# Optimization experiments

Hardware: AMD Instinct MI355X
Metric: run time of the kernel (lower is better)

## Reference

```python
import jax, jax.numpy as jnp
import numpy as np

N = 100000
E = 1600000
F_IN = 32
HID = 16


def _sage_conv(x, src, dst, W_l, b_l, W_r):
    # PyG SAGEConv (aggr='mean', normalize=False, root_weight=True):
    #   out = lin_l(mean_{j in N(i)} x_j) + lin_r(x_i)
    # lin_l has bias, lin_r has no bias.
    n = x.shape[0]
    msg_sum = jax.ops.segment_sum(x[src], dst, num_segments=n)          # [N, d]
    deg = jax.ops.segment_sum(jnp.ones_like(dst, dtype=x.dtype), dst, num_segments=n)
    agg = msg_sum / jnp.maximum(deg, 1.0)[:, None]                      # mean, 0 for isolated nodes
    return agg @ W_l.T + b_l + x @ W_r.T


def setup_inputs() -> dict:
    key = jax.random.key(0)
    ks = jax.random.split(key, 8)
    x = jax.random.normal(ks[0], (N, F_IN), dtype=jnp.float32)
    edge_index = jax.random.randint(ks[1], (1, 2, E), 0, N, dtype=jnp.int64)
    s1 = 1.0 / np.sqrt(F_IN)
    s2 = 1.0 / np.sqrt(HID)
    W1_l = jax.random.uniform(ks[2], (HID, F_IN), jnp.float32, -s1, s1)
    b1_l = jax.random.uniform(ks[3], (HID,), jnp.float32, -s1, s1)
    W1_r = jax.random.uniform(ks[4], (HID, F_IN), jnp.float32, -s1, s1)
    W2_l = jax.random.uniform(ks[5], (F_IN, HID), jnp.float32, -s2, s2)
    b2_l = jax.random.uniform(ks[6], (F_IN,), jnp.float32, -s2, s2)
    W2_r = jax.random.uniform(ks[7], (F_IN, HID), jnp.float32, -s2, s2)
    return {"x": x, "edge_index": edge_index, "W1_l": W1_l, "b1_l": b1_l,
            "W1_r": W1_r, "W2_l": W2_l, "b2_l": b2_l, "W2_r": W2_r}


def reference(x, edge_index, W1_l, b1_l, W1_r, W2_l, b2_l, W2_r):
    ei = jnp.squeeze(edge_index, axis=0)  # [2, E]
    src, dst = ei[0], ei[1]
    h = jax.nn.relu(_sage_conv(x, src, dst, W1_l, b1_l, W1_r))
    out = _sage_conv(h, src, dst, W2_l, b2_l, W2_r)
    return out
```

## Files before the change

kernel.cpp:

```cpp
#include <hip/hip_runtime.h>

#define F_IN 32
#define HID 16
#define BSHIFT 7
#define BNODES (1 << BSHIFT)
#define CAP 2560
#define CHUNK 8192
#define SRCM 0x1FFFFu
#define WS1 33
#define WS2 17

__device__ __forceinline__ void add4(float4& a, const float4& b) {
    a.x += b.x; a.y += b.y; a.z += b.z; a.w += b.w;
}
__device__ __forceinline__ unsigned pack2(float a, float b) {
    unsigned ua = __float_as_uint(a);
    unsigned ub = __float_as_uint(b);
    ua = (ua + 0x7FFFu + ((ua >> 16) & 1u)) >> 16;
    ub = (ub + 0x7FFFu + ((ub >> 16) & 1u)) >> 16;
    return ua | (ub << 16);
}
__device__ __forceinline__ float lo2f(unsigned u) { return __uint_as_float(u << 16); }
__device__ __forceinline__ float hi2f(unsigned u) { return __uint_as_float(u & 0xFFFF0000u); }
__device__ __forceinline__ float4 unp(uint2 v) {
    return make_float4(lo2f(v.x), hi2f(v.x), lo2f(v.y), hi2f(v.y));
}

__global__ void __launch_bounds__(256) k_pre(const float* __restrict__ x,
                                             const float* __restrict__ W1_l,
                                             unsigned* __restrict__ y1b,
                                             const int* __restrict__ ei,
                                             int* __restrict__ bucketCursor,
                                             unsigned* __restrict__ bucketBuf,
                                             int N, int E, int nodeBlocks) {
    __shared__ int cnt[1024];
    __shared__ int runBase[1024];
    __shared__ float Ws[HID * F_IN];
    int tid = threadIdx.x;

    if ((int)blockIdx.x < nodeBlocks) {
        for (int i = tid; i < HID * F_IN; i += 256) Ws[i] = W1_l[i];
        __syncthreads();
        int node = blockIdx.x * 256 + tid;
        if (node >= N) return;
        float xr[F_IN];
        const float4* xp = (const float4*)(x + (size_t)node * F_IN);
#pragma unroll
        for (int i = 0; i < F_IN / 4; i++) {
            float4 v = xp[i];
            xr[4 * i + 0] = v.x; xr[4 * i + 1] = v.y;
            xr[4 * i + 2] = v.z; xr[4 * i + 3] = v.w;
        }
        float a[HID];
#pragma unroll
        for (int o = 0; o < HID; o++) {
            float s = 0.f;
#pragma unroll
            for (int k = 0; k < F_IN; k++) s += xr[k] * Ws[o * F_IN + k];
            a[o] = s;
        }
        uint4* yp = (uint4*)(y1b + (size_t)node * 8);
        yp[0] = make_uint4(pack2(a[0], a[1]), pack2(a[2], a[3]),
                           pack2(a[4], a[5]), pack2(a[6], a[7]));
        yp[1] = make_uint4(pack2(a[8], a[9]), pack2(a[10], a[11]),
                           pack2(a[12], a[13]), pack2(a[14], a[15]));
        return;
    }

    int pb = blockIdx.x - nodeBlocks;
    int e0 = pb * CHUNK;
    int e1 = min(e0 + CHUNK, E);
    int n4 = (e1 - e0) >> 2;
    const int4* dst4 = (const int4*)(ei + E + e0);
    const int4* src4 = (const int4*)(ei + e0);

#pragma unroll
    for (int i = 0; i < 4; i++) cnt[tid + 256 * i] = 0;
    __syncthreads();
    for (int i = tid; i < n4; i += 256) {
        int4 d = dst4[i];
        atomicAdd(&cnt[d.x >> BSHIFT], 1);
        atomicAdd(&cnt[d.y >> BSHIFT], 1);
        atomicAdd(&cnt[d.z >> BSHIFT], 1);
        atomicAdd(&cnt[d.w >> BSHIFT], 1);
    }
    __syncthreads();
#pragma unroll
    for (int i = 0; i < 4; i++) {
        int b = tid + 256 * i;
        int c = cnt[b];
        runBase[b] = c ? atomicAdd(&bucketCursor[b], c) : 0;
        cnt[b] = 0;
    }
    __syncthreads();
    for (int i = tid; i < n4; i += 256) {
        int4 d = dst4[i];
        int4 s = src4[i];
        {
            int b = d.x >> BSHIFT;
            int pos = runBase[b] + atomicAdd(&cnt[b], 1);
            if (pos < CAP)
                bucketBuf[(size_t)b * CAP + pos] = ((unsigned)(d.x & (BNODES - 1)) << 17) | (unsigned)s.x;
        }
        {
            int b = d.y >> BSHIFT;
            int pos = runBase[b] + atomicAdd(&cnt[b], 1);
            if (pos < CAP)
                bucketBuf[(size_t)b * CAP + pos] = ((unsigned)(d.y & (BNODES - 1)) << 17) | (unsigned)s.y;
        }
        {
            int b = d.z >> BSHIFT;
            int pos = runBase[b] + atomicAdd(&cnt[b], 1);
            if (pos < CAP)
                bucketBuf[(size_t)b * CAP + pos] = ((unsigned)(d.z & (BNODES - 1)) << 17) | (unsigned)s.z;
        }
        {
            int b = d.w >> BSHIFT;
            int pos = runBase[b] + atomicAdd(&cnt[b], 1);
            if (pos < CAP)
                bucketBuf[(size_t)b * CAP + pos] = ((unsigned)(d.w & (BNODES - 1)) << 17) | (unsigned)s.w;
        }
    }
}

__global__ void __launch_bounds__(256) k_agg1f(const unsigned* __restrict__ y1b,
                                               const float* __restrict__ x,
                                               const unsigned* __restrict__ bucketBuf,
                                               const int* __restrict__ bucketCursor,
                                               const float* __restrict__ W1_r,
                                               const float* __restrict__ b1,
                                               unsigned* __restrict__ hb, int N) {
    __shared__ unsigned sA[CAP];
    __shared__ unsigned sB[CAP];
    __shared__ int hist[BNODES];
    __shared__ int scn[BNODES];
    __shared__ int cur[BNODES];
    __shared__ float Ws[HID * WS1];
    __shared__ float bs[HID];
    int tid = threadIdx.x, b = blockIdx.x;

    for (int i = tid; i < HID * F_IN; i += 256) Ws[(i >> 5) * WS1 + (i & 31)] = W1_r[i];
    if (tid < HID) bs[tid] = b1[tid];
    if (tid < BNODES) hist[tid] = 0;
    int nRec = min(bucketCursor[b], CAP);
    const unsigned* buf = bucketBuf + (size_t)b * CAP;
    for (int i = tid; i < nRec; i += 256) sA[i] = buf[i];
    __syncthreads();
    for (int i = tid; i < nRec; i += 256) atomicAdd(&hist[sA[i] >> 17], 1);
    __syncthreads();
    if (tid < BNODES) scn[tid] = hist[tid];
    __syncthreads();
    for (int off = 1; off < BNODES; off <<= 1) {
        int v = (tid < BNODES && tid >= off) ? scn[tid - off] : 0;
        __syncthreads();
        if (tid < BNODES && tid >= off) scn[tid] += v;
        __syncthreads();
    }
    if (tid < BNODES) cur[tid] = scn[tid] - hist[tid];
    __syncthreads();
    for (int i = tid; i < nRec; i += 256) {
        unsigned r = sA[i];
        int pos = atomicAdd(&cur[r >> 17], 1);
        sB[pos] = r & SRCM;
    }
    __syncthreads();

    const uint2* yv = (const uint2*)y1b;
#pragma unroll
    for (int pass = 0; pass < 2; pass++) {
        int slot = pass * 256 + tid;
        int nl = slot >> 2, c = slot & 3;
        int node = b * BNODES + nl;
        if (node >= N) continue;
        int start = scn[nl] - hist[nl];
        int dg = hist[nl];
        int jend = start + dg;
        float4 a0 = make_float4(0, 0, 0, 0), a1 = a0;
        int j = start;
        for (; j + 4 <= jend; j += 4) {
            unsigned s0 = sB[j], s1 = sB[j + 1], s2 = sB[j + 2], s3 = sB[j + 3];
            uint2 v0 = yv[(size_t)s0 * 4 + c];
            uint2 v1 = yv[(size_t)s1 * 4 + c];
            uint2 v2 = yv[(size_t)s2 * 4 + c];
            uint2 v3 = yv[(size_t)s3 * 4 + c];
            add4(a0, unp(v0)); add4(a1, unp(v1));
            add4(a0, unp(v2)); add4(a1, unp(v3));
        }
        for (; j < jend; j++) {
            uint2 v = yv[(size_t)sB[j] * 4 + c];
            add4(a0, unp(v));
        }
        add4(a0, a1);
        float inv = 1.0f / (float)(dg > 0 ? dg : 1);
        float m[4] = {a0.x * inv, a0.y * inv, a0.z * inv, a0.w * inv};

        float xr[F_IN];
        const float4* xp = (const float4*)(x + (size_t)node * F_IN);
#pragma unroll
        for (int q = 0; q < F_IN / 4; q++) {
            float4 v = xp[q];
            xr[4 * q + 0] = v.x; xr[4 * q + 1] = v.y;
            xr[4 * q + 2] = v.z; xr[4 * q + 3] = v.w;
        }
        float a[4];
#pragma unroll
        for (int jj = 0; jj < 4; jj++) {
            int o = c * 4 + jj;
            float s = m[jj] + bs[o];
#pragma unroll
            for (int k = 0; k < F_IN; k++) s += xr[k] * Ws[o * WS1 + k];
            a[jj] = fmaxf(s, 0.0f);
        }
        ((uint2*)hb)[(size_t)node * 4 + c] = make_uint2(pack2(a[0], a[1]), pack2(a[2], a[3]));
    }
}

__global__ void __launch_bounds__(256) k_l2f(const unsigned* __restrict__ hb,
                                             const unsigned* __restrict__ bucketBuf,
                                             const int* __restrict__ bucketCursor,
                                             const float* __restrict__ W2_l,
                                             const float* __restrict__ b2,
                                             const float* __restrict__ W2_r,
                                             float* __restrict__ out, int N) {
    __shared__ unsigned sA[CAP];
    __shared__ unsigned sB[CAP];
    __shared__ int hist[BNODES];
    __shared__ int scn[BNODES];
    __shared__ int cur[BNODES];
    __shared__ float Wl[F_IN * WS2];
    __shared__ float Wr[F_IN * WS2];
    __shared__ float bs[F_IN];
    int tid = threadIdx.x, b = blockIdx.x;

    for (int i = tid; i < F_IN * HID; i += 256) {
        int r = i >> 4, q = i & 15;
        Wl[r * WS2 + q] = W2_l[i];
        Wr[r * WS2 + q] = W2_r[i];
    }
    if (tid < F_IN) bs[tid] = b2[tid];
    if (tid < BNODES) hist[tid] = 0;
    int nRec = min(bucketCursor[b], CAP);
    const unsigned* buf = bucketBuf + (size_t)b * CAP;
    for (int i = tid; i < nRec; i += 256) sA[i] = buf[i];
    __syncthreads();
    for (int i = tid; i < nRec; i += 256) atomicAdd(&hist[sA[i] >> 17], 1);
    __syncthreads();
    if (tid < BNODES) scn[tid] = hist[tid];
    __syncthreads();
    for (int off = 1; off < BNODES; off <<= 1) {
        int v = (tid < BNODES && tid >= off) ? scn[tid - off] : 0;
        __syncthreads();
        if (tid < BNODES && tid >= off) scn[tid] += v;
        __syncthreads();
    }
    if (tid < BNODES) cur[tid] = scn[tid] - hist[tid];
    __syncthreads();
    for (int i = tid; i < nRec; i += 256) {
        unsigned r = sA[i];
        int pos = atomicAdd(&cur[r >> 17], 1);
        sB[pos] = r & SRCM;
    }
    __syncthreads();

    float* mm = (float*)sA;
    const uint2* hv = (const uint2*)hb;
#pragma unroll
    for (int pass = 0; pass < 2; pass++) {
        int slot = pass * 256 + tid;
        int nl = slot >> 2, c = slot & 3;
        int node = b * BNODES + nl;
        if (node >= N) continue;
        int start = scn[nl] - hist[nl];
        int dg = hist[nl];
        int jend = start + dg;
        float4 a0 = make_float4(0, 0, 0, 0), a1 = a0;
        int j = start;
        for (; j + 4 <= jend; j += 4) {
            unsigned s0 = sB[j], s1 = sB[j + 1], s2 = sB[j + 2], s3 = sB[j + 3];
            uint2 v0 = hv[(size_t)s0 * 4 + c];
            uint2 v1 = hv[(size_t)s1 * 4 + c];
            uint2 v2 = hv[(size_t)s2 * 4 + c];
            uint2 v3 = hv[(size_t)s3 * 4 + c];
            add4(a0, unp(v0)); add4(a1, unp(v1));
            add4(a0, unp(v2)); add4(a1, unp(v3));
        }
        for (; j < jend; j++) {
            uint2 v = hv[(size_t)sB[j] * 4 + c];
            add4(a0, unp(v));
        }
        add4(a0, a1);
        float inv = 1.0f / (float)(dg > 0 ? dg : 1);
        mm[nl * (HID + 1) + c * 4 + 0] = a0.x * inv;
        mm[nl * (HID + 1) + c * 4 + 1] = a0.y * inv;
        mm[nl * (HID + 1) + c * 4 + 2] = a0.z * inv;
        mm[nl * (HID + 1) + c * 4 + 3] = a0.w * inv;
    }
    __syncthreads();

#pragma unroll
    for (int pass = 0; pass < 2; pass++) {
        int slot = pass * 256 + tid;
        int nl = slot >> 2, c = slot & 3;
        int node = b * BNODES + nl;
        if (node >= N) continue;

        float m[HID];
#pragma unroll
        for (int k = 0; k < HID; k++) m[k] = mm[nl * (HID + 1) + k];

        float hr[HID];
        const uint4* hp = (const uint4*)(hb + (size_t)node * 8);
        uint4 u0 = hp[0], u1 = hp[1];
        hr[0] = lo2f(u0.x); hr[1] = hi2f(u0.x); hr[2] = lo2f(u0.y); hr[3] = hi2f(u0.y);
        hr[4] = lo2f(u0.z); hr[5] = hi2f(u0.z); hr[6] = lo2f(u0.w); hr[7] = hi2f(u0.w);
        hr[8] = lo2f(u1.x); hr[9] = hi2f(u1.x); hr[10] = lo2f(u1.y); hr[11] = hi2f(u1.y);
        hr[12] = lo2f(u1.z); hr[13] = hi2f(u1.z); hr[14] = lo2f(u1.w); hr[15] = hi2f(u1.w);

        float a[8];
#pragma unroll
        for (int jj = 0; jj < 8; jj++) {
            int o = c * 8 + jj;
            float s = bs[o];
#pragma unroll
            for (int k = 0; k < HID; k++)
                s += m[k] * Wl[o * WS2 + k] + hr[k] * Wr[o * WS2 + k];
            a[jj] = s;
        }
        float4* op = (float4*)(out + (size_t)node * F_IN + c * 8);
        op[0] = make_float4(a[0], a[1], a[2], a[3]);
        op[1] = make_float4(a[4], a[5], a[6], a[7]);
    }
}

extern "C" void kernel_launch(void* const* d_in, const int* in_sizes, int n_in,
                              void* d_out, int out_size, void* d_ws, size_t ws_size,
                              hipStream_t stream) {
    const float* x    = (const float*)d_in[0];
    const int*   ei   = (const int*)d_in[1];
    const float* W1_l = (const float*)d_in[2];
    const float* b1   = (const float*)d_in[3];
    const float* W1_r = (const float*)d_in[4];
    const float* W2_l = (const float*)d_in[5];
    const float* b2   = (const float*)d_in[6];
    const float* W2_r = (const float*)d_in[7];
    float* out = (float*)d_out;

    const int N = in_sizes[0] / F_IN;
    const int E = in_sizes[1] / 2;
    const int nbuckets = (N + BNODES - 1) >> BSHIFT;

    int* bucketCursor = (int*)d_ws;
    unsigned* bucketBuf = (unsigned*)(bucketCursor + 1024);
    unsigned* y1b = bucketBuf + (size_t)nbuckets * CAP;
    unsigned* hb  = y1b + (size_t)N * 8;

    hipMemsetAsync(bucketCursor, 0, 1024 * sizeof(int), stream);

    const int nodeBlocks = (N + 255) / 256;
    const int partBlocks = (E + CHUNK - 1) / CHUNK;

    k_pre<<<nodeBlocks + partBlocks, 256, 0, stream>>>(x, W1_l, y1b, ei,
                                                       bucketCursor, bucketBuf,
                                                       N, E, nodeBlocks);
    k_agg1f<<<nbuckets, 256, 0, stream>>>(y1b, x, bucketBuf, bucketCursor,
                                          W1_r, b1, hb, N);
    k_l2f<<<nbuckets, 256, 0, stream>>>(hb, bucketBuf, bucketCursor,
                                        W2_l, b2, W2_r, out, N);
}
```

Before: 159.9 us.

## Reuse layer-1 CSR sort in layer 2, split dense matvecs across lanes, unroll gathers

```diff
diff --git a/kernel.cpp b/kernel.cpp
--- a/kernel.cpp
+++ b/kernel.cpp
@@ -5,7 +5,7 @@
 #define BSHIFT 7
 #define BNODES (1 << BSHIFT)
 #define CAP 2560
-#define CHUNK 8192
+#define CHUNK 4096
 #define SRCM 0x1FFFFu
 #define WS1 33
 #define WS2 17
@@ -125,8 +125,9 @@
 
 __global__ void __launch_bounds__(256) k_agg1f(const unsigned* __restrict__ y1b,
                                                const float* __restrict__ x,
-                                               const unsigned* __restrict__ bucketBuf,
+                                               unsigned* __restrict__ bucketBuf,
                                                const int* __restrict__ bucketCursor,
+                                               unsigned* __restrict__ rdPacked,
                                                const float* __restrict__ W1_r,
                                                const float* __restrict__ b1,
                                                unsigned* __restrict__ hb, int N) {
@@ -143,7 +144,7 @@
     if (tid < HID) bs[tid] = b1[tid];
     if (tid < BNODES) hist[tid] = 0;
     int nRec = min(bucketCursor[b], CAP);
-    const unsigned* buf = bucketBuf + (size_t)b * CAP;
+    unsigned* buf = bucketBuf + (size_t)b * CAP;
     for (int i = tid; i < nRec; i += 256) sA[i] = buf[i];
     __syncthreads();
     for (int i = tid; i < nRec; i += 256) atomicAdd(&hist[sA[i] >> 17], 1);
@@ -164,6 +165,13 @@
         sB[pos] = r & SRCM;
     }
     __syncthreads();
+
+    for (int i = tid; i < nRec; i += 256) buf[i] = sB[i];
+    if (tid < BNODES) {
+        int node = b * BNODES + tid;
+        if (node < N)
+            rdPacked[node] = ((unsigned)(scn[tid] - hist[tid]) << 16) | (unsigned)hist[tid];
+    }
 
     const uint2* yv = (const uint2*)y1b;
 #pragma unroll
@@ -175,41 +183,53 @@
         int start = scn[nl] - hist[nl];
         int dg = hist[nl];
         int jend = start + dg;
-        float4 a0 = make_float4(0, 0, 0, 0), a1 = a0;
+        float4 a0 = make_float4(0, 0, 0, 0), a1 = a0, a2 = a0, a3 = a0;
         int j = start;
-        for (; j + 4 <= jend; j += 4) {
+        for (; j + 8 <= jend; j += 8) {
             unsigned s0 = sB[j], s1 = sB[j + 1], s2 = sB[j + 2], s3 = sB[j + 3];
+            unsigned s4 = sB[j + 4], s5 = sB[j + 5], s6 = sB[j + 6], s7 = sB[j + 7];
             uint2 v0 = yv[(size_t)s0 * 4 + c];
             uint2 v1 = yv[(size_t)s1 * 4 + c];
             uint2 v2 = yv[(size_t)s2 * 4 + c];
             uint2 v3 = yv[(size_t)s3 * 4 + c];
-            add4(a0, unp(v0)); add4(a1, unp(v1));
-            add4(a0, unp(v2)); add4(a1, unp(v3));
+            uint2 v4 = yv[(size_t)s4 * 4 + c];
+            uint2 v5 = yv[(size_t)s5 * 4 + c];
+            uint2 v6 = yv[(size_t)s6 * 4 + c];
+            uint2 v7 = yv[(size_t)s7 * 4 + c];
+            add4(a0, unp(v0)); add4(a1, unp(v1)); add4(a2, unp(v2)); add4(a3, unp(v3));
+            add4(a0, unp(v4)); add4(a1, unp(v5)); add4(a2, unp(v6)); add4(a3, unp(v7));
         }
         for (; j < jend; j++) {
             uint2 v = yv[(size_t)sB[j] * 4 + c];
             add4(a0, unp(v));
         }
-        add4(a0, a1);
+        add4(a0, a1); add4(a2, a3); add4(a0, a2);
         float inv = 1.0f / (float)(dg > 0 ? dg : 1);
         float m[4] = {a0.x * inv, a0.y * inv, a0.z * inv, a0.w * inv};
 
-        float xr[F_IN];
-        const float4* xp = (const float4*)(x + (size_t)node * F_IN);
-#pragma unroll
-        for (int q = 0; q < F_IN / 4; q++) {
-            float4 v = xp[q];
-            xr[4 * q + 0] = v.x; xr[4 * q + 1] = v.y;
-            xr[4 * q + 2] = v.z; xr[4 * q + 3] = v.w;
+        float xq[8];
+        const float4* xp = (const float4*)(x + (size_t)node * F_IN + c * 8);
+        float4 va = xp[0], vb = xp[1];
+        xq[0] = va.x; xq[1] = va.y; xq[2] = va.z; xq[3] = va.w;
+        xq[4] = vb.x; xq[5] = vb.y; xq[6] = vb.z; xq[7] = vb.w;
+        float p[HID];
+#pragma unroll
+        for (int o = 0; o < HID; o++) {
+            float s = 0.f;
+#pragma unroll
+            for (int k = 0; k < 8; k++) s += xq[k] * Ws[o * WS1 + c * 8 + k];
+            p[o] = s;
+        }
+#pragma unroll
+        for (int o = 0; o < HID; o++) {
+            p[o] += __shfl_xor(p[o], 1);
+            p[o] += __shfl_xor(p[o], 2);
         }
         float a[4];
 #pragma unroll
         for (int jj = 0; jj < 4; jj++) {
             int o = c * 4 + jj;
-            float s = m[jj] + bs[o];
-#pragma unroll
-            for (int k = 0; k < F_IN; k++) s += xr[k] * Ws[o * WS1 + k];
-            a[jj] = fmaxf(s, 0.0f);
+            a[jj] = fmaxf(m[jj] + bs[o] + p[o], 0.0f);
         }
         ((uint2*)hb)[(size_t)node * 4 + c] = make_uint2(pack2(a[0], a[1]), pack2(a[2], a[3]));
     }
@@ -218,15 +238,14 @@
 __global__ void __launch_bounds__(256) k_l2f(const unsigned* __restrict__ hb,
                                              const unsigned* __restrict__ bucketBuf,
                                              const int* __restrict__ bucketCursor,
+                                             const unsigned* __restrict__ rdPacked,
                                              const float* __restrict__ W2_l,
                                              const float* __restrict__ b2,
                                              const float* __restrict__ W2_r,
                                              float* __restrict__ out, int N) {
-    __shared__ unsigned sA[CAP];
     __shared__ unsigned sB[CAP];
-    __shared__ int hist[BNODES];
-    __shared__ int scn[BNODES];
-    __shared__ int cur[BNODES];
+    __shared__ float mm[BNODES * (HID + 1)];
+    __shared__ unsigned rdS[BNODES];
     __shared__ float Wl[F_IN * WS2];
     __shared__ float Wr[F_IN * WS2];
     __shared__ float bs[F_IN];
@@ -238,31 +257,15 @@
         Wr[r * WS2 + q] = W2_r[i];
     }
     if (tid < F_IN) bs[tid] = b2[tid];
-    if (tid < BNODES) hist[tid] = 0;
     int nRec = min(bucketCursor[b], CAP);
     const unsigned* buf = bucketBuf + (size_t)b * CAP;
-    for (int i = tid; i < nRec; i += 256) sA[i] = buf[i];
-    __syncthreads();
-    for (int i = tid; i < nRec; i += 256) atomicAdd(&hist[sA[i] >> 17], 1);
-    __syncthreads();
-    if (tid < BNODES) scn[tid] = hist[tid];
-    __syncthreads();
-    for (int off = 1; off < BNODES; off <<= 1) {
-        int v = (tid < BNODES && tid >= off) ? scn[tid - off] : 0;
-        __syncthreads();
-        if (tid < BNODES && tid >= off) scn[tid] += v;
-        __syncthreads();
-    }
-    if (tid < BNODES) cur[tid] = scn[tid] - hist[tid];
-    __syncthreads();
-    for (int i = tid; i < nRec; i += 256) {
-        unsigned r = sA[i];
-        int pos = atomicAdd(&cur[r >> 17], 1);
-        sB[pos] = r & SRCM;
-    }
-    __syncthreads();
-
-    float* mm = (float*)sA;
+    for (int i = tid; i < nRec; i += 256) sB[i] = buf[i];
+    if (tid < BNODES) {
+        int node = b * BNODES + tid;
+        rdS[tid] = (node < N) ? rdPacked[node] : 0u;
+    }
+    __syncthreads();
+
     const uint2* hv = (const uint2*)hb;
 #pragma unroll
     for (int pass = 0; pass < 2; pass++) {
@@ -270,25 +273,31 @@
         int nl = slot >> 2, c = slot & 3;
         int node = b * BNODES + nl;
         if (node >= N) continue;
-        int start = scn[nl] - hist[nl];
-        int dg = hist[nl];
+        unsigned rd = rdS[nl];
+        int start = rd >> 16;
+        int dg = rd & 0xFFFFu;
         int jend = start + dg;
-        float4 a0 = make_float4(0, 0, 0, 0), a1 = a0;
+        float4 a0 = make_float4(0, 0, 0, 0), a1 = a0, a2 = a0, a3 = a0;
         int j = start;
-        for (; j + 4 <= jend; j += 4) {
+        for (; j + 8 <= jend; j += 8) {
             unsigned s0 = sB[j], s1 = sB[j + 1], s2 = sB[j + 2], s3 = sB[j + 3];
+            unsigned s4 = sB[j + 4], s5 = sB[j + 5], s6 = sB[j + 6], s7 = sB[j + 7];
             uint2 v0 = hv[(size_t)s0 * 4 + c];
             uint2 v1 = hv[(size_t)s1 * 4 + c];
             uint2 v2 = hv[(size_t)s2 * 4 + c];
             uint2 v3 = hv[(size_t)s3 * 4 + c];
-            add4(a0, unp(v0)); add4(a1, unp(v1));
-            add4(a0, unp(v2)); add4(a1, unp(v3));
+            uint2 v4 = hv[(size_t)s4 * 4 + c];
+            uint2 v5 = hv[(size_t)s5 * 4 + c];
+            uint2 v6 = hv[(size_t)s6 * 4 + c];
+            uint2 v7 = hv[(size_t)s7 * 4 + c];
+            add4(a0, unp(v0)); add4(a1, unp(v1)); add4(a2, unp(v2)); add4(a3, unp(v3));
+            add4(a0, unp(v4)); add4(a1, unp(v5)); add4(a2, unp(v6)); add4(a3, unp(v7));
         }
         for (; j < jend; j++) {
             uint2 v = hv[(size_t)sB[j] * 4 + c];
             add4(a0, unp(v));
         }
-        add4(a0, a1);
+        add4(a0, a1); add4(a2, a3); add4(a0, a2);
         float inv = 1.0f / (float)(dg > 0 ? dg : 1);
         mm[nl * (HID + 1) + c * 4 + 0] = a0.x * inv;
         mm[nl * (HID + 1) + c * 4 + 1] = a0.y * inv;
@@ -304,31 +313,43 @@
         int node = b * BNODES + nl;
         if (node >= N) continue;
 
-        float m[HID];
-#pragma unroll
-        for (int k = 0; k < HID; k++) m[k] = mm[nl * (HID + 1) + k];
-
-        float hr[HID];
-        const uint4* hp = (const uint4*)(hb + (size_t)node * 8);
-        uint4 u0 = hp[0], u1 = hp[1];
-        hr[0] = lo2f(u0.x); hr[1] = hi2f(u0.x); hr[2] = lo2f(u0.y); hr[3] = hi2f(u0.y);
-        hr[4] = lo2f(u0.z); hr[5] = hi2f(u0.z); hr[6] = lo2f(u0.w); hr[7] = hi2f(u0.w);
-        hr[8] = lo2f(u1.x); hr[9] = hi2f(u1.x); hr[10] = lo2f(u1.y); hr[11] = hi2f(u1.y);
-        hr[12] = lo2f(u1.z); hr[13] = hi2f(u1.z); hr[14] = lo2f(u1.w); hr[15] = hi2f(u1.w);
-
-        float a[8];
-#pragma unroll
-        for (int jj = 0; jj < 8; jj++) {
-            int o = c * 8 + jj;
-            float s = bs[o];
-#pragma unroll
-            for (int k = 0; k < HID; k++)
-                s += m[k] * Wl[o * WS2 + k] + hr[k] * Wr[o * WS2 + k];
-            a[jj] = s;
+        float hq[4];
+        uint2 hv2 = ((const uint2*)hb)[(size_t)node * 4 + c];
+        float4 hf = unp(hv2);
+        hq[0] = hf.x; hq[1] = hf.y; hq[2] = hf.z; hq[3] = hf.w;
+        float mq[4];
+#pragma unroll
+        for (int k = 0; k < 4; k++) mq[k] = mm[nl * (HID + 1) + c * 4 + k];
+
+        float aout[8];
+#pragma unroll
+        for (int half = 0; half < 2; half++) {
+            float p[16];
+#pragma unroll
+            for (int jj = 0; jj < 16; jj++) {
+                int o = half * 16 + jj;
+                float s = 0.f;
+#pragma unroll
+                for (int k = 0; k < 4; k++)
+                    s += mq[k] * Wl[o * WS2 + c * 4 + k] + hq[k] * Wr[o * WS2 + c * 4 + k];
+                p[jj] = s;
+            }
+#pragma unroll
+            for (int jj = 0; jj < 16; jj++) {
+                p[jj] += __shfl_xor(p[jj], 1);
+                p[jj] += __shfl_xor(p[jj], 2);
+            }
+            if ((c >> 1) == half) {
+#pragma unroll
+                for (int jj = 0; jj < 8; jj++) {
+                    int o = c * 8 + jj;
+                    aout[jj] = bs[o] + p[o - half * 16];
+                }
+            }
         }
         float4* op = (float4*)(out + (size_t)node * F_IN + c * 8);
-        op[0] = make_float4(a[0], a[1], a[2], a[3]);
-        op[1] = make_float4(a[4], a[5], a[6], a[7]);
+        op[0] = make_float4(aout[0], aout[1], aout[2], aout[3]);
+        op[1] = make_float4(aout[4], aout[5], aout[6], aout[7]);
     }
 }
 
@@ -351,7 +372,8 @@
 
     int* bucketCursor = (int*)d_ws;
     unsigned* bucketBuf = (unsigned*)(bucketCursor + 1024);
-    unsigned* y1b = bucketBuf + (size_t)nbuckets * CAP;
+    unsigned* rdPacked = bucketBuf + (size_t)nbuckets * CAP;
+    unsigned* y1b = rdPacked + N;
     unsigned* hb  = y1b + (size_t)N * 8;
 
     hipMemsetAsync(bucketCursor, 0, 1024 * sizeof(int), stream);
@@ -363,7 +385,7 @@
                                                        bucketCursor, bucketBuf,
                                                        N, E, nodeBlocks);
     k_agg1f<<<nbuckets, 256, 0, stream>>>(y1b, x, bucketBuf, bucketCursor,
-                                          W1_r, b1, hb, N);
-    k_l2f<<<nbuckets, 256, 0, stream>>>(hb, bucketBuf, bucketCursor,
+                                          rdPacked, W1_r, b1, hb, N);
+    k_l2f<<<nbuckets, 256, 0, stream>>>(hb, bucketBuf, bucketCursor, rdPacked,
                                         W2_l, b2, W2_r, out, N);
 }
```

Result: no change. 163.0 us (+1.9%).
